# Optimization experiments

Measured on AMD Instinct MI355X. Metric: run time of the kernel, lower is better.

The kernel has to match this reference:

```python
import jax, jax.numpy as jnp
import numpy as np

B, N, D_OBJ, D_Q, D_FUSED, D_BOX, D_ATT = 64, 36, 2048, 2048, 2048, 4, 512


def setup_inputs() -> dict:
    key = jax.random.key(0)
    ks = jax.random.split(key, 12)
    s = lambda d: 1.0 / np.sqrt(d)
    return {
        "question_embedding": jax.random.normal(ks[0], (B * N, D_Q), jnp.float32),
        "object_features_list": jax.random.normal(ks[1], (B, N, D_OBJ), jnp.float32),
        "bounding_boxes": jax.random.uniform(ks[2], (B, N, D_BOX), jnp.float32),
        "Wq": jax.random.normal(ks[3], (D_Q, D_FUSED), jnp.float32) * s(D_Q),
        "Wo": jax.random.normal(ks[4], (D_OBJ, D_FUSED), jnp.float32) * s(D_OBJ),
        "Wfa": jax.random.normal(ks[5], (D_FUSED, D_FUSED), jnp.float32) * s(D_FUSED),
        "Wfb": jax.random.normal(ks[6], (D_FUSED, D_FUSED), jnp.float32) * s(D_FUSED),
        "Wba": jax.random.normal(ks[7], (D_BOX, D_FUSED), jnp.float32) * s(D_BOX),
        "Wbb": jax.random.normal(ks[8], (D_BOX, D_FUSED), jnp.float32) * s(D_BOX),
        "W0": jax.random.normal(ks[9], (D_FUSED, D_ATT), jnp.float32) * s(D_FUSED),
        "b0": jnp.zeros((D_ATT,), jnp.float32),
        "W1": jax.random.normal(ks[10], (D_ATT, 1), jnp.float32) * s(D_ATT),
        "b1": jnp.zeros((1,), jnp.float32),
        "batch_size": B,
        "num_obj": N,
    }


def reference(question_embedding, object_features_list, bounding_boxes,
              Wq, Wo, Wfa, Wfb, Wba, Wbb, W0, b0, W1, b1,
              batch_size, num_obj):
    # fuse_object_features_with_questions: MLB fusion of question and objects
    obj_flat = object_features_list.reshape(batch_size * num_obj, -1)  # [BN, D]
    fused = (question_embedding @ Wq) * (obj_flat @ Wo)                # [BN, Df]
    fused = fused.reshape(batch_size, num_obj, -1)                     # [B, N, Df]

    # pairwise: project once, broadcast-multiply instead of materializing
    # expanded [B*N*N, D] operands (same math as expand+view+fusion).
    ra = fused @ Wfa                 # [B, N, Df]
    rb = fused @ Wfb                 # [B, N, Df]
    ba = bounding_boxes @ Wba        # [B, N, Df]
    bb = bounding_boxes @ Wbb        # [B, N, Df]
    # relations[b, i, j, :] = fusion_fused(f_i, f_j) + fusion_box(box_i, box_j)
    relations = ra[:, :, None, :] * rb[:, None, :, :] + ba[:, :, None, :] * bb[:, None, :, :]  # [B,N,N,Df]

    # compute_relation_attention: linear-tanh-linear, softmax over dim=2
    h = jnp.tanh(relations @ W0 + b0)          # [B, N, N, D_att]
    scores = h @ W1 + b1                       # [B, N, N, 1]
    att = jax.nn.softmax(scores, axis=2)[..., 0]  # [B, N, N]
    e_hat = jnp.sum(relations * att[..., None], axis=2)  # [B, N, Df]

    pairwise_res = fused + e_hat
    return object_features_list + pairwise_res
```

## Files before the change

### kernel.cpp

```cpp
#include <hip/hip_runtime.h>
#include <hip/hip_bf16.h>
#include <math.h>

constexpr int kB    = 64;
constexpr int kN    = 36;
constexpr int kBN   = kB * kN;
constexpr int kD    = 2048;
constexpr int kDatt = 512;
constexpr int kPairs = kN * kN;

using bf16x8 = __attribute__((ext_vector_type(8))) short;
using f32x4  = __attribute__((ext_vector_type(4))) float;

typedef unsigned int u32;
typedef __attribute__((address_space(3))) u32 lds_u32;
typedef const __attribute__((address_space(1))) u32 glb_u32;

__device__ inline unsigned short f2bf(float f) {
    union { float f; unsigned u; } v; v.f = f;
    unsigned r = v.u + 0x7FFFu + ((v.u >> 16) & 1u);
    return (unsigned short)(r >> 16);
}

__global__ __launch_bounds__(256)
void kcvt(const float* __restrict__ x, unsigned short* __restrict__ y, int n4)
{
    int i = blockIdx.x * 256 + threadIdx.x;
    if (i < n4) {
        float4 v = ((const float4*)x)[i];
        ushort4 o = {f2bf(v.x), f2bf(v.y), f2bf(v.z), f2bf(v.w)};
        ((ushort4*)y)[i] = o;
    }
}

__global__ __launch_bounds__(256)
void ktrp(const float* __restrict__ W, unsigned short* __restrict__ WT, int nt)
{
    __shared__ float T[64][65];
    const int k0 = blockIdx.x * 64;
    const int n0 = blockIdx.y * 64;
    const int c = threadIdx.x & 63, r0 = threadIdx.x >> 6;
    #pragma unroll
    for (int rr = 0; rr < 64; rr += 4)
        T[r0 + rr][c] = W[(size_t)(k0 + r0 + rr) * nt + n0 + c];
    __syncthreads();
    #pragma unroll
    for (int rr = 0; rr < 64; rr += 4)
        WT[(size_t)(n0 + r0 + rr) * kD + k0 + c] = f2bf(T[c][r0 + rr]);
}

__global__ __launch_bounds__(256)
void k3_box_proj(const float* __restrict__ box, const float* __restrict__ Wba,
                 const float* __restrict__ Wbb,
                 float* __restrict__ ba, float* __restrict__ bb)
{
    const int r = blockIdx.y;
    const int c = blockIdx.x * 256 + threadIdx.x;
    const float x0 = box[r * 4 + 0], x1 = box[r * 4 + 1];
    const float x2 = box[r * 4 + 2], x3 = box[r * 4 + 3];
    float va = x0 * Wba[c] + x1 * Wba[kD + c] + x2 * Wba[2 * kD + c] + x3 * Wba[3 * kD + c];
    float vb = x0 * Wbb[c] + x1 * Wbb[kD + c] + x2 * Wbb[2 * kD + c] + x3 * Wbb[3 * kD + c];
    ba[(size_t)r * kD + c] = va;
    bb[(size_t)r * kD + c] = vb;
}

__device__ inline void stage128(const unsigned short* __restrict__ g,
                                int grow0, int k0,
                                unsigned short* lds, int w, int lane)
{
    const int sr = lane >> 2, sc = (lane & 3) * 8;
    #pragma unroll
    for (int t = 0; t < 2; ++t) {
        int r = w * 32 + t * 16;
        const unsigned short* gp = g + (size_t)(grow0 + r + sr) * kD + k0 + sc;
        __builtin_amdgcn_global_load_lds((glb_u32*)gp, (lds_u32*)(lds + r * 32), 16, 0, 0);
    }
}
__device__ inline void stage64(const unsigned short* __restrict__ g,
                               int grow0, int k0,
                               unsigned short* lds, int w, int lane)
{
    const int sr = lane >> 2, sc = (lane & 3) * 8;
    int r = w * 16;
    const unsigned short* gp = g + (size_t)(grow0 + r + sr) * kD + k0 + sc;
    __builtin_amdgcn_global_load_lds((glb_u32*)gp, (lds_u32*)(lds + r * 32), 16, 0, 0);
}

__global__ __launch_bounds__(256, 2)
void k1_dual_mfma(const unsigned short* __restrict__ Qb,
                  const unsigned short* __restrict__ WqT,
                  const unsigned short* __restrict__ Ob,
                  const unsigned short* __restrict__ WoT,
                  unsigned short* __restrict__ fusedb)
{
    __shared__ __align__(16) unsigned short As1[128][32];
    __shared__ __align__(16) unsigned short As2[128][32];
    __shared__ __align__(16) unsigned short Bs1[64][32];
    __shared__ __align__(16) unsigned short Bs2[64][32];

    const int tid = threadIdx.x;
    const int lane = tid & 63;
    const int w = tid >> 6;
    const int wm = w >> 1, wn = w & 1;
    const int row0 = blockIdx.y * 128;
    const int col0 = blockIdx.x * 64;

    f32x4 acc1[4][2], acc2[4][2];
    #pragma unroll
    for (int mt = 0; mt < 4; ++mt)
        #pragma unroll
        for (int nt = 0; nt < 2; ++nt) { acc1[mt][nt] = (f32x4)(0.f); acc2[mt][nt] = (f32x4)(0.f); }

    const int fr = lane & 15, ko = (lane >> 4) * 8;

    for (int k0 = 0; k0 < kD; k0 += 32) {
        stage128(Qb,  row0, k0, &As1[0][0], w, lane);
        stage128(Ob,  row0, k0, &As2[0][0], w, lane);
        stage64 (WqT, col0, k0, &Bs1[0][0], w, lane);
        stage64 (WoT, col0, k0, &Bs2[0][0], w, lane);
        __syncthreads();

        bf16x8 a1[4], a2[4];
        #pragma unroll
        for (int mt = 0; mt < 4; ++mt) {
            a1[mt] = *(bf16x8*)&As1[wm * 64 + mt * 16 + fr][ko];
            a2[mt] = *(bf16x8*)&As2[wm * 64 + mt * 16 + fr][ko];
        }
        #pragma unroll
        for (int nt = 0; nt < 2; ++nt) {
            bf16x8 b1 = *(bf16x8*)&Bs1[wn * 32 + nt * 16 + fr][ko];
            bf16x8 b2 = *(bf16x8*)&Bs2[wn * 32 + nt * 16 + fr][ko];
            #pragma unroll
            for (int mt = 0; mt < 4; ++mt) {
                acc1[mt][nt] = __builtin_amdgcn_mfma_f32_16x16x32_bf16(a1[mt], b1, acc1[mt][nt], 0, 0, 0);
                acc2[mt][nt] = __builtin_amdgcn_mfma_f32_16x16x32_bf16(a2[mt], b2, acc2[mt][nt], 0, 0, 0);
            }
        }
        __syncthreads();
    }

    const int fq = lane >> 4;
    #pragma unroll
    for (int mt = 0; mt < 4; ++mt)
        #pragma unroll
        for (int nt = 0; nt < 2; ++nt) {
            int row = row0 + wm * 64 + mt * 16 + fq * 4;
            int col = col0 + wn * 32 + nt * 16 + fr;
            #pragma unroll
            for (int reg = 0; reg < 4; ++reg) {
                float v = acc1[mt][nt][reg] * acc2[mt][nt][reg];
                fusedb[(size_t)(row + reg) * kD + col] = f2bf(v);
            }
        }
}

__global__ __launch_bounds__(256, 2)
void k2_dual_mfma(const unsigned short* __restrict__ Fb,
                  const unsigned short* __restrict__ WfaT,
                  const unsigned short* __restrict__ WfbT,
                  float* __restrict__ ra, float* __restrict__ rb)
{
    __shared__ __align__(16) unsigned short As [128][32];
    __shared__ __align__(16) unsigned short Bs1[64][32];
    __shared__ __align__(16) unsigned short Bs2[64][32];

    const int tid = threadIdx.x;
    const int lane = tid & 63;
    const int w = tid >> 6;
    const int wm = w >> 1, wn = w & 1;
    const int row0 = blockIdx.y * 128;
    const int col0 = blockIdx.x * 64;

    f32x4 acc1[4][2], acc2[4][2];
    #pragma unroll
    for (int mt = 0; mt < 4; ++mt)
        #pragma unroll
        for (int nt = 0; nt < 2; ++nt) { acc1[mt][nt] = (f32x4)(0.f); acc2[mt][nt] = (f32x4)(0.f); }

    const int fr = lane & 15, ko = (lane >> 4) * 8;

    for (int k0 = 0; k0 < kD; k0 += 32) {
        stage128(Fb,   row0, k0, &As [0][0], w, lane);
        stage64 (WfaT, col0, k0, &Bs1[0][0], w, lane);
        stage64 (WfbT, col0, k0, &Bs2[0][0], w, lane);
        __syncthreads();

        bf16x8 a[4];
        #pragma unroll
        for (int mt = 0; mt < 4; ++mt)
            a[mt] = *(bf16x8*)&As[wm * 64 + mt * 16 + fr][ko];
        #pragma unroll
        for (int nt = 0; nt < 2; ++nt) {
            bf16x8 b1 = *(bf16x8*)&Bs1[wn * 32 + nt * 16 + fr][ko];
            bf16x8 b2 = *(bf16x8*)&Bs2[wn * 32 + nt * 16 + fr][ko];
            #pragma unroll
            for (int mt = 0; mt < 4; ++mt) {
                acc1[mt][nt] = __builtin_amdgcn_mfma_f32_16x16x32_bf16(a[mt], b1, acc1[mt][nt], 0, 0, 0);
                acc2[mt][nt] = __builtin_amdgcn_mfma_f32_16x16x32_bf16(a[mt], b2, acc2[mt][nt], 0, 0, 0);
            }
        }
        __syncthreads();
    }

    const int fq = lane >> 4;
    #pragma unroll
    for (int mt = 0; mt < 4; ++mt)
        #pragma unroll
        for (int nt = 0; nt < 2; ++nt) {
            int row = row0 + wm * 64 + mt * 16 + fq * 4;
            int col = col0 + wn * 32 + nt * 16 + fr;
            #pragma unroll
            for (int reg = 0; reg < 4; ++reg) {
                size_t o = (size_t)(row + reg) * kD + col;
                ra[o] = acc1[mt][nt][reg];
                rb[o] = acc2[mt][nt][reg];
            }
        }
}

__global__ __launch_bounds__(512, 2)
void k4_scores_mfma(const float* __restrict__ ra, const float* __restrict__ rb,
                    const float* __restrict__ ba, const float* __restrict__ bb,
                    const unsigned short* __restrict__ W0T,
                    const float* __restrict__ b0, const float* __restrict__ W1,
                    float* __restrict__ scores)
{
    __shared__ __align__(16) unsigned short Bs[2][512][32];
    __shared__ __align__(16) unsigned short RelS[2][128][40];
    __shared__ float scoreS[128];

    const int tid  = threadIdx.x;
    const int lane = tid & 63;
    const int w    = tid >> 6;
    const int wm   = w >> 2;
    const int wn   = w & 3;
    const int b    = blockIdx.y;
    const int m0   = blockIdx.x * 128;

    int rowA[2], cgA[2];
    const float *raP[2], *rbP[2], *baP[2], *bbP[2];
    #pragma unroll
    for (int t = 0; t < 2; ++t) {
        int s = tid + t * 512;
        rowA[t] = s >> 3; cgA[t] = s & 7;
        int p = m0 + rowA[t]; if (p >= kPairs) p = kPairs - 1;
        int i = p / 36, j = p - i * 36;
        raP[t] = ra + (size_t)(b * 36 + i) * kD;
        baP[t] = ba + (size_t)(b * 36 + i) * kD;
        rbP[t] = rb + (size_t)(b * 36 + j) * kD;
        bbP[t] = bb + (size_t)(b * 36 + j) * kD;
    }

    const int fr = lane & 15, fq = lane >> 4;
    const int sr = lane >> 2, sc = (lane & 3) * 8;

    f32x4 acc[4][8];
    #pragma unroll
    for (int mt = 0; mt < 4; ++mt)
        #pragma unroll
        for (int nt = 0; nt < 8; ++nt)
            acc[mt][nt] = (f32x4)(0.f);

    if (tid < 128) scoreS[tid] = 0.f;

    float4 pa[2], pr[2], pp[2], pq[2];

    #define ISSUE_B(k0_, buf_)                                                   \
        _Pragma("unroll")                                                        \
        for (int t = 0; t < 4; ++t) {                                            \
            int r0 = w * 64 + t * 16;                                            \
            const unsigned short* gp = W0T + (size_t)(r0 + sr) * kD + (k0_) + sc;\
            __builtin_amdgcn_global_load_lds((glb_u32*)gp,                       \
                (lds_u32*)&Bs[buf_][r0][0], 16, 0, 0);                           \
        }

    #define LOAD_A(k0_)                                                          \
        _Pragma("unroll")                                                        \
        for (int t = 0; t < 2; ++t) {                                            \
            pa[t] = *(const float4*)(raP[t] + (k0_) + cgA[t] * 4);               \
            pr[t] = *(const float4*)(rbP[t] + (k0_) + cgA[t] * 4);               \
            pp[t] = *(const float4*)(baP[t] + (k0_) + cgA[t] * 4);               \
            pq[t] = *(const float4*)(bbP[t] + (k0_) + cgA[t] * 4);               \
        }

    #define WRITE_REL(buf_)                                                      \
        _Pragma("unroll")                                                        \
        for (int t = 0; t < 2; ++t) {                                            \
            ushort4 o;                                                           \
            o.x = f2bf(pa[t].x * pr[t].x + pp[t].x * pq[t].x);                   \
            o.y = f2bf(pa[t].y * pr[t].y + pp[t].y * pq[t].y);                   \
            o.z = f2bf(pa[t].z * pr[t].z + pp[t].z * pq[t].z);                   \
            o.w = f2bf(pa[t].w * pr[t].w + pp[t].w * pq[t].w);                   \
            *(ushort4*)&RelS[buf_][rowA[t]][cgA[t] * 4] = o;                     \
        }

    ISSUE_B(0, 0)
    LOAD_A(0)
    WRITE_REL(0)

    for (int k0 = 0; k0 < kD; k0 += 32) {
        const int cur = (k0 >> 5) & 1, nxt = cur ^ 1;
        const bool more = (k0 + 32 < kD);
        __syncthreads();
        if (more) {
            ISSUE_B(k0 + 32, nxt)
            LOAD_A(k0 + 32)
        }
        bf16x8 af[4];
        #pragma unroll
        for (int mt = 0; mt < 4; ++mt)
            af[mt] = *(bf16x8*)&RelS[cur][wm * 64 + mt * 16 + fr][fq * 8];
        #pragma unroll
        for (int nt = 0; nt < 8; ++nt) {
            bf16x8 bf = *(bf16x8*)&Bs[cur][wn * 128 + nt * 16 + fr][fq * 8];
            #pragma unroll
            for (int mt = 0; mt < 4; ++mt)
                acc[mt][nt] = __builtin_amdgcn_mfma_f32_16x16x32_bf16(af[mt], bf, acc[mt][nt], 0, 0, 0);
        }
        if (more) { WRITE_REL(nxt) }
    }

    float b0v[8], w1v[8];
    #pragma unroll
    for (int nt = 0; nt < 8; ++nt) {
        int col = wn * 128 + nt * 16 + fr;
        b0v[nt] = b0[col];
        w1v[nt] = W1[col];
    }
    #pragma unroll
    for (int mt = 0; mt < 4; ++mt) {
        #pragma unroll
        for (int reg = 0; reg < 4; ++reg) {
            float p = 0.f;
            #pragma unroll
            for (int nt = 0; nt < 8; ++nt)
                p += w1v[nt] * tanhf(acc[mt][nt][reg] + b0v[nt]);
            p += __shfl_xor(p, 1, 64);
            p += __shfl_xor(p, 2, 64);
            p += __shfl_xor(p, 4, 64);
            p += __shfl_xor(p, 8, 64);
            if (fr == 0)
                atomicAdd(&scoreS[wm * 64 + mt * 16 + fq * 4 + reg], p);
        }
    }
    __syncthreads();
    if (tid < 128 && m0 + tid < kPairs)
        scores[(size_t)b * kPairs + m0 + tid] = scoreS[tid];
}

__global__ __launch_bounds__(64)
void k5_softmax(const float* __restrict__ scores, float* __restrict__ att)
{
    const int bi = blockIdx.x;
    const int tid = threadIdx.x;
    float s = (tid < kN) ? scores[(size_t)bi * kN + tid] : -1e30f;
    float m = s;
    #pragma unroll
    for (int off = 32; off >= 1; off >>= 1)
        m = fmaxf(m, __shfl_xor(m, off, 64));
    float e = (tid < kN) ? expf(s - m) : 0.f;
    float sum = e;
    #pragma unroll
    for (int off = 32; off >= 1; off >>= 1)
        sum += __shfl_xor(sum, off, 64);
    if (tid < kN) att[(size_t)bi * kN + tid] = e / sum;
}

__global__ __launch_bounds__(256)
void k6_output(const float* __restrict__ obj, const unsigned short* __restrict__ fusedb,
               const float* __restrict__ ra, const float* __restrict__ ba,
               const float* __restrict__ rb, const float* __restrict__ bb,
               const float* __restrict__ att, float* __restrict__ out)
{
    __shared__ float attS[kN];
    const int bi = blockIdx.x;
    const int b = bi / kN;
    const int tid = threadIdx.x;
    if (tid < kN) attS[tid] = att[(size_t)bi * kN + tid];
    __syncthreads();
    for (int d = tid; d < kD; d += 256) {
        float s1 = 0.f, s2 = 0.f;
        #pragma unroll 4
        for (int j = 0; j < kN; ++j) {
            float a = attS[j];
            size_t rrow = (size_t)(b * kN + j) * kD + d;
            s1 = fmaf(a, rb[rrow], s1);
            s2 = fmaf(a, bb[rrow], s2);
        }
        size_t o = (size_t)bi * kD + d;
        float fv = __uint_as_float((u32)fusedb[o] << 16);
        out[o] = obj[o] + fv + ra[o] * s1 + ba[o] * s2;
    }
}

extern "C" void kernel_launch(void* const* d_in, const int* in_sizes, int n_in,
                              void* d_out, int out_size, void* d_ws, size_t ws_size,
                              hipStream_t stream)
{
    const float* q   = (const float*)d_in[0];
    const float* obj = (const float*)d_in[1];
    const float* box = (const float*)d_in[2];
    const float* Wq  = (const float*)d_in[3];
    const float* Wo  = (const float*)d_in[4];
    const float* Wfa = (const float*)d_in[5];
    const float* Wfb = (const float*)d_in[6];
    const float* Wba = (const float*)d_in[7];
    const float* Wbb = (const float*)d_in[8];
    const float* W0  = (const float*)d_in[9];
    const float* b0v = (const float*)d_in[10];
    const float* W1  = (const float*)d_in[11];
    float* out = (float*)d_out;

    const size_t nBD = (size_t)kBN * kD;
    float* ws = (float*)d_ws;
    size_t off = 0;
    float* ra     = ws + off; off += nBD;
    float* rb     = ws + off; off += nBD;
    float* ba     = ws + off; off += nBD;
    float* bb     = ws + off; off += nBD;
    float* scores = ws + off; off += (size_t)kBN * kN;
    float* att    = ws + off; off += (size_t)kBN * kN;

    unsigned short* us = (unsigned short*)(ws + off);
    size_t uoff = 0;
    unsigned short* W0T     = us + uoff; uoff += (size_t)kDatt * kD;
    unsigned short* q_bf    = us + uoff; uoff += nBD;
    unsigned short* obj_bf  = us + uoff; uoff += nBD;
    unsigned short* fusedbf = us + uoff; uoff += nBD;
    unsigned short* WqT     = us + uoff; uoff += (size_t)kD * kD;
    unsigned short* WoT     = us + uoff; uoff += (size_t)kD * kD;
    unsigned short* WfaT = q_bf;
    unsigned short* WfbT = obj_bf;

    const int n4 = (int)(nBD / 4);
    kcvt<<<dim3((n4 + 255) / 256), 256, 0, stream>>>(q,   q_bf,   n4);
    kcvt<<<dim3((n4 + 255) / 256), 256, 0, stream>>>(obj, obj_bf, n4);
    ktrp<<<dim3(32, 32), 256, 0, stream>>>(Wq, WqT, kD);
    ktrp<<<dim3(32, 32), 256, 0, stream>>>(Wo, WoT, kD);
    ktrp<<<dim3(32, 8),  256, 0, stream>>>(W0, W0T, kDatt);
    k3_box_proj<<<dim3(kD / 256, kBN), 256, 0, stream>>>(box, Wba, Wbb, ba, bb);

    k1_dual_mfma<<<dim3(kD / 64, kBN / 128), 256, 0, stream>>>(q_bf, WqT, obj_bf, WoT, fusedbf);

    ktrp<<<dim3(32, 32), 256, 0, stream>>>(Wfa, WfaT, kD);
    ktrp<<<dim3(32, 32), 256, 0, stream>>>(Wfb, WfbT, kD);

    k2_dual_mfma<<<dim3(kD / 64, kBN / 128), 256, 0, stream>>>(fusedbf, WfaT, WfbT, ra, rb);

    k4_scores_mfma<<<dim3(11, kB), 512, 0, stream>>>(ra, rb, ba, bb, W0T, b0v, W1, scores);
    k5_softmax<<<kBN, 64, 0, stream>>>(scores, att);
    k6_output<<<kBN, 256, 0, stream>>>(obj, fusedbf, ra, ba, rb, bb, att, out);
}
```

Baseline: 766.0 us.

## Flatten pair-score grid across batches and swizzle W0 LDS layout

The scores kernel now tiles over the flattened batch*pair rows (kRows/128 blocks) instead of 11 blocks per batch, so tiles are no longer padded to 1408 rows per batch. The W0T tile is stored in LDS with a permuted row/column mapping meant to cut bank conflicts on the bf16x8 fragment reads. Activation loads are also issued before the async B loads. Tiles can now straddle two batches, so the address math gets a little more complex.

```diff
diff --git a/kernel.cpp b/kernel.cpp
--- a/kernel.cpp
+++ b/kernel.cpp
@@ -8,6 +8,7 @@
 constexpr int kD    = 2048;
 constexpr int kDatt = 512;
 constexpr int kPairs = kN * kN;
+constexpr int kRows  = kB * kPairs;
 
 using bf16x8 = __attribute__((ext_vector_type(8))) short;
 using f32x4  = __attribute__((ext_vector_type(4))) float;
@@ -225,7 +226,7 @@
                     const float* __restrict__ b0, const float* __restrict__ W1,
                     float* __restrict__ scores)
 {
-    __shared__ __align__(16) unsigned short Bs[2][512][32];
+    __shared__ __align__(16) unsigned short Bs[2][512 * 32];
     __shared__ __align__(16) unsigned short RelS[2][128][40];
     __shared__ float scoreS[128];
 
@@ -234,8 +235,7 @@
     const int w    = tid >> 6;
     const int wm   = w >> 2;
     const int wn   = w & 3;
-    const int b    = blockIdx.y;
-    const int m0   = blockIdx.x * 128;
+    const int t0   = blockIdx.x * 128;
 
     int rowA[2], cgA[2];
     const float *raP[2], *rbP[2], *baP[2], *bbP[2];
@@ -243,16 +243,20 @@
     for (int t = 0; t < 2; ++t) {
         int s = tid + t * 512;
         rowA[t] = s >> 3; cgA[t] = s & 7;
-        int p = m0 + rowA[t]; if (p >= kPairs) p = kPairs - 1;
-        int i = p / 36, j = p - i * 36;
-        raP[t] = ra + (size_t)(b * 36 + i) * kD;
-        baP[t] = ba + (size_t)(b * 36 + i) * kD;
-        rbP[t] = rb + (size_t)(b * 36 + j) * kD;
-        bbP[t] = bb + (size_t)(b * 36 + j) * kD;
+        int gp = t0 + rowA[t];
+        int b  = gp / kPairs;
+        int r  = gp - b * kPairs;
+        int i  = r / kN, j = r - i * kN;
+        raP[t] = ra + (size_t)(b * kN + i) * kD;
+        baP[t] = ba + (size_t)(b * kN + i) * kD;
+        rbP[t] = rb + (size_t)(b * kN + j) * kD;
+        bbP[t] = bb + (size_t)(b * kN + j) * kD;
     }
 
     const int fr = lane & 15, fq = lane >> 4;
-    const int sr = lane >> 2, sc = (lane & 3) * 8;
+    const int bsr = (lane & 7) + ((lane >> 5) << 3);
+    const int bsc = ((lane >> 3) & 3) * 8;
+    const int bco = ((fr & 7) << 3) + ((fr >> 3) << 8) + (fq << 6);
 
     f32x4 acc[4][8];
     #pragma unroll
@@ -269,9 +273,9 @@
         _Pragma("unroll")                                                        \
         for (int t = 0; t < 4; ++t) {                                            \
             int r0 = w * 64 + t * 16;                                            \
-            const unsigned short* gp = W0T + (size_t)(r0 + sr) * kD + (k0_) + sc;\
+            const unsigned short* gp = W0T + (size_t)(r0 + bsr) * kD + (k0_) + bsc;\
             __builtin_amdgcn_global_load_lds((glb_u32*)gp,                       \
-                (lds_u32*)&Bs[buf_][r0][0], 16, 0, 0);                           \
+                (lds_u32*)&Bs[buf_][r0 * 32], 16, 0, 0);                         \
         }
 
     #define LOAD_A(k0_)                                                          \
@@ -294,8 +298,8 @@
             *(ushort4*)&RelS[buf_][rowA[t]][cgA[t] * 4] = o;                     \
         }
 
+    LOAD_A(0)
     ISSUE_B(0, 0)
-    LOAD_A(0)
     WRITE_REL(0)
 
     for (int k0 = 0; k0 < kD; k0 += 32) {
@@ -303,8 +307,8 @@
         const bool more = (k0 + 32 < kD);
         __syncthreads();
         if (more) {
+            LOAD_A(k0 + 32)
             ISSUE_B(k0 + 32, nxt)
-            LOAD_A(k0 + 32)
         }
         bf16x8 af[4];
         #pragma unroll
@@ -312,10 +316,10 @@
             af[mt] = *(bf16x8*)&RelS[cur][wm * 64 + mt * 16 + fr][fq * 8];
         #pragma unroll
         for (int nt = 0; nt < 8; ++nt) {
-            bf16x8 bf = *(bf16x8*)&Bs[cur][wn * 128 + nt * 16 + fr][fq * 8];
+            bf16x8 bfv = *(bf16x8*)&Bs[cur][wn * 4096 + nt * 512 + bco];
             #pragma unroll
             for (int mt = 0; mt < 4; ++mt)
-                acc[mt][nt] = __builtin_amdgcn_mfma_f32_16x16x32_bf16(af[mt], bf, acc[mt][nt], 0, 0, 0);
+                acc[mt][nt] = __builtin_amdgcn_mfma_f32_16x16x32_bf16(af[mt], bfv, acc[mt][nt], 0, 0, 0);
         }
         if (more) { WRITE_REL(nxt) }
     }
@@ -344,8 +348,8 @@
         }
     }
     __syncthreads();
-    if (tid < 128 && m0 + tid < kPairs)
-        scores[(size_t)b * kPairs + m0 + tid] = scoreS[tid];
+    if (tid < 128)
+        scores[(size_t)t0 + tid] = scoreS[tid];
 }
 
 __global__ __launch_bounds__(64)
@@ -447,7 +451,7 @@
 
     k2_dual_mfma<<<dim3(kD / 64, kBN / 128), 256, 0, stream>>>(fusedbf, WfaT, WfbT, ra, rb);
 
-    k4_scores_mfma<<<dim3(11, kB), 512, 0, stream>>>(ra, rb, ba, bb, W0T, b0v, W1, scores);
+    k4_scores_mfma<<<dim3(kRows / 128), 512, 0, stream>>>(ra, rb, ba, bb, W0T, b0v, W1, scores);
     k5_softmax<<<kBN, 64, 0, stream>>>(scores, att);
     k6_output<<<kBN, 256, 0, stream>>>(obj, fusedbf, ra, ba, rb, bb, att, out);
 }
```

Measured after the change: 856.1 us. 1.12x slower.
